# Kernel optimization log

Measured on AMD Instinct MI355X. Metric: run time of the kernel, lower is better.

Reference implementation:

```python
import jax, jax.numpy as jnp
import numpy as np

L = 0.05  # lx = ly = lz box half-extent

# 8 box corners [8,3]
_CORNERS = jnp.array([[sx * L, sy * L, sz * L]
                      for sx in (-1.0, 1.0) for sy in (-1.0, 1.0) for sz in (-1.0, 1.0)],
                     dtype=jnp.float32)
# match original ordering: [-,-,-],[-,-,+],[-,+,-],... which the comprehension above yields


def _euler_R(pose):
    """pose: [B,6] -> R [B,3,3], t [B,3] (yaw, pitch, roll convention from source)."""
    yaw, pitch, roll = pose[:, 0], pose[:, 1], pose[:, 2]
    cy, sy = jnp.cos(yaw), jnp.sin(yaw)
    cp, sp = jnp.cos(pitch), jnp.sin(pitch)
    cr, sr = jnp.cos(roll), jnp.sin(roll)
    R = jnp.stack([
        jnp.stack([cy * cp, cy * sp * sr - sy * cr, cy * sp * cr + sy * sr], axis=-1),
        jnp.stack([sy * cp, sy * sp * sr + cy * cr, sy * sp * cr - cy * sr], axis=-1),
        jnp.stack([-sp, cp * sr, cp * cr], axis=-1),
    ], axis=-2)  # [B,3,3]
    t = pose[:, 3:]  # [B,3]
    return R, t


def _transform_corners(pose):
    R, t = _euler_R(pose)
    # [B,8,3] = corners @ R^T + t
    return jnp.einsum('bij,nj->bni', R, _CORNERS) + t[:, None, :]


def setup_inputs() -> dict:
    key = jax.random.key(0)
    k1, k2, k3, k4 = jax.random.split(key, 4)
    B, C = 1048576, 16
    return {
        'pred_pose': jax.random.normal(k1, (B, 6), dtype=jnp.float32),
        'pred_class': jax.random.normal(k2, (B, C), dtype=jnp.float32),
        'target_pose': jax.random.normal(k3, (B, 6), dtype=jnp.float32),
        'target_class': jax.random.normal(k4, (B, C), dtype=jnp.float32),
    }


def reference(pred_pose, pred_class, target_pose, target_class):
    pts_pred = _transform_corners(pred_pose)    # [B,8,3]
    pts_gt = _transform_corners(target_pose)    # [B,8,3]
    # per-sample pose diff: mean over 8 corner L2 norms, then mean over batch
    norms = jnp.linalg.norm(pts_pred - pts_gt, axis=-1)  # [B,8]
    loss_pose = norms.mean(axis=-1).mean()
    class_loss = jnp.mean((pred_class - target_class) ** 2)
    total_loss = loss_pose + class_loss
    return total_loss, loss_pose, class_loss
```

## Files before the change

### kernel.cpp

```cpp
#include <hip/hip_runtime.h>
#include <math.h>

#define CORNER_L 0.05f

typedef float f4 __attribute__((ext_vector_type(4)));

constexpr int THREADS = 256;
constexpr int GROUPS  = 1024;
constexpr int CQ = 3, PQ = 2;
constexpr int CBLOCKS = CQ * GROUPS;
constexpr int PBLOCKS = PQ * GROUPS;
constexpr int TOTAL_BLOCKS = CBLOCKS + PBLOCKS;

__device__ __forceinline__ float pose_elem(
    float py, float pp_, float pr, float ptx, float pty, float ptz,
    float ty, float tp_, float tr, float ttx, float tty, float ttz)
{
    float sy1 = __sinf(py),  cy1 = __cosf(py);
    float sp1 = __sinf(pp_), cp1 = __cosf(pp_);
    float sr1 = __sinf(pr),  cr1 = __cosf(pr);
    float sy2 = __sinf(ty),  cy2 = __cosf(ty);
    float sp2 = __sinf(tp_), cp2 = __cosf(tp_);
    float sr2 = __sinf(tr),  cr2 = __cosf(tr);

    float a0 = CORNER_L * (cy1 * cp1 - cy2 * cp2);
    float a1 = CORNER_L * ((cy1 * sp1 * sr1 - sy1 * cr1) - (cy2 * sp2 * sr2 - sy2 * cr2));
    float a2 = CORNER_L * ((cy1 * sp1 * cr1 + sy1 * sr1) - (cy2 * sp2 * cr2 + sy2 * sr2));
    float b0 = CORNER_L * (sy1 * cp1 - sy2 * cp2);
    float b1 = CORNER_L * ((sy1 * sp1 * sr1 + cy1 * cr1) - (sy2 * sp2 * sr2 + cy2 * cr2));
    float b2 = CORNER_L * ((sy1 * sp1 * cr1 - cy1 * sr1) - (sy2 * sp2 * cr2 - cy2 * sr2));
    float c0 = CORNER_L * (sp2 - sp1);
    float c1 = CORNER_L * (cp1 * sr1 - cp2 * sr2);
    float c2 = CORNER_L * (cp1 * cr1 - cp2 * cr2);
    float dtx = ptx - ttx;
    float dty = pty - tty;
    float dtz = ptz - ttz;

    float nsum = 0.0f;
    #pragma unroll
    for (int s = 0; s < 8; ++s) {
        float sx = (s & 4) ? 1.0f : -1.0f;
        float sy = (s & 2) ? 1.0f : -1.0f;
        float sz = (s & 1) ? 1.0f : -1.0f;
        float d0 = sx * a0 + sy * a1 + sz * a2 + dtx;
        float d1 = sx * b0 + sy * b1 + sz * b2 + dty;
        float d2 = sx * c0 + sy * c1 + sz * c2 + dtz;
        nsum += __builtin_amdgcn_sqrtf(d0 * d0 + d1 * d1 + d2 * d2);
    }
    return nsum;
}

__global__ __launch_bounds__(THREADS) void pose_loss_fused(
    const f4* __restrict__ pp4, const f4* __restrict__ pc4,
    const f4* __restrict__ tp4, const f4* __restrict__ tc4,
    float* __restrict__ ws, int n4)
{
    const int tid = threadIdx.x;
    const int g   = blockIdx.x;
    const int grp = g / 5;
    const int r   = g - grp * 5;

    float acc = 0.0f;
    int out_idx;

    if (r < CQ) {
        const int cb = grp * CQ + r;
        const size_t G = (size_t)CBLOCKS * THREADS;
        for (size_t i = (size_t)cb * THREADS + tid; i < (size_t)n4; i += G) {
            f4 p = __builtin_nontemporal_load(pc4 + i);
            f4 t = __builtin_nontemporal_load(tc4 + i);
            f4 d = p - t;
            acc += d.x * d.x + d.y * d.y + d.z * d.z + d.w * d.w;
        }
        out_idx = cb;
    } else {
        const int pb = grp * PQ + (r - CQ);
        const size_t gtid = (size_t)pb * THREADS + tid;
        const size_t f = gtid * 3;
        f4 P0 = __builtin_nontemporal_load(pp4 + f);
        f4 P1 = __builtin_nontemporal_load(pp4 + f + 1);
        f4 P2 = __builtin_nontemporal_load(pp4 + f + 2);
        f4 T0 = __builtin_nontemporal_load(tp4 + f);
        f4 T1 = __builtin_nontemporal_load(tp4 + f + 1);
        f4 T2 = __builtin_nontemporal_load(tp4 + f + 2);
        acc += pose_elem(P0.x, P0.y, P0.z, P0.w, P1.x, P1.y,
                         T0.x, T0.y, T0.z, T0.w, T1.x, T1.y);
        acc += pose_elem(P1.z, P1.w, P2.x, P2.y, P2.z, P2.w,
                         T1.z, T1.w, T2.x, T2.y, T2.z, T2.w);
        out_idx = CBLOCKS + pb;
    }

    #pragma unroll
    for (int off = 32; off > 0; off >>= 1) acc += __shfl_down(acc, off);
    __shared__ float red[4];
    const int lane = tid & 63, wave = tid >> 6;
    if (lane == 0) red[wave] = acc;
    __syncthreads();
    if (tid == 0) ws[out_idx] = red[0] + red[1] + red[2] + red[3];
}

__global__ __launch_bounds__(THREADS) void pose_loss_finalize(
    const float* __restrict__ ws, float* __restrict__ out,
    float inv_pose, float inv_class)
{
    float c = 0.0f, p = 0.0f;
    for (int k = threadIdx.x; k < CBLOCKS; k += THREADS) c += ws[k];
    for (int k = threadIdx.x; k < PBLOCKS; k += THREADS) p += ws[CBLOCKS + k];
    #pragma unroll
    for (int off = 32; off > 0; off >>= 1) {
        p += __shfl_down(p, off);
        c += __shfl_down(c, off);
    }
    __shared__ float r_p[4], r_c[4];
    const int lane = threadIdx.x & 63, wave = threadIdx.x >> 6;
    if (lane == 0) { r_p[wave] = p; r_c[wave] = c; }
    __syncthreads();
    if (threadIdx.x == 0) {
        float lp = (r_p[0] + r_p[1] + r_p[2] + r_p[3]) * inv_pose;
        float lc = (r_c[0] + r_c[1] + r_c[2] + r_c[3]) * inv_class;
        out[0] = lp + lc;
        out[1] = lp;
        out[2] = lc;
    }
}

extern "C" void kernel_launch(void* const* d_in, const int* in_sizes, int n_in,
                              void* d_out, int out_size, void* d_ws, size_t ws_size,
                              hipStream_t stream) {
    const f4* pred_pose    = (const f4*)d_in[0];
    const f4* pred_class   = (const f4*)d_in[1];
    const f4* target_pose  = (const f4*)d_in[2];
    const f4* target_class = (const f4*)d_in[3];
    float* out = (float*)d_out;
    float* ws  = (float*)d_ws;

    const int B  = in_sizes[0] / 6;
    const int n4 = B * 4;

    pose_loss_fused<<<TOTAL_BLOCKS, THREADS, 0, stream>>>(
        pred_pose, pred_class, target_pose, target_class, ws, n4);

    const float inv_pose  = 1.0f / (8.0f  * (float)B);
    const float inv_class = 1.0f / (16.0f * (float)B);
    pose_loss_finalize<<<1, THREADS, 0, stream>>>(ws, out, inv_pose, inv_class);
}
```

Measured before the change: 174.6 us.

## Fuse finalize into main kernel via last-block atomic counter, unroll class loop

Removes the separate finalize kernel launch: each block writes its partial sum, fences, and bumps an atomic counter, and the last block to arrive does the final reduction and writes the outputs. A memset resets the counter before each launch. The class-loss loop is also unrolled by two with independent accumulators to get more loads in flight. The change trades one kernel launch for a memset op, an atomic per block and a serialized tail in the last block.

After: 425.8 us. +143.8%, slower.

```diff
diff --git a/kernel.cpp b/kernel.cpp
--- a/kernel.cpp
+++ b/kernel.cpp
@@ -53,7 +53,8 @@
 __global__ __launch_bounds__(THREADS) void pose_loss_fused(
     const f4* __restrict__ pp4, const f4* __restrict__ pc4,
     const f4* __restrict__ tp4, const f4* __restrict__ tc4,
-    float* __restrict__ ws, int n4)
+    float* __restrict__ ws, float* __restrict__ out,
+    int n4, float inv_pose, float inv_class)
 {
     const int tid = threadIdx.x;
     const int g   = blockIdx.x;
@@ -66,12 +67,20 @@
     if (r < CQ) {
         const int cb = grp * CQ + r;
         const size_t G = (size_t)CBLOCKS * THREADS;
-        for (size_t i = (size_t)cb * THREADS + tid; i < (size_t)n4; i += G) {
-            f4 p = __builtin_nontemporal_load(pc4 + i);
-            f4 t = __builtin_nontemporal_load(tc4 + i);
-            f4 d = p - t;
-            acc += d.x * d.x + d.y * d.y + d.z * d.z + d.w * d.w;
+        float acc1 = 0.0f;
+        for (size_t i = (size_t)cb * THREADS + tid; i < (size_t)n4; i += 2 * G) {
+            f4 p0 = __builtin_nontemporal_load(pc4 + i);
+            f4 t0 = __builtin_nontemporal_load(tc4 + i);
+            if (i + G < (size_t)n4) {
+                f4 p1 = __builtin_nontemporal_load(pc4 + i + G);
+                f4 t1 = __builtin_nontemporal_load(tc4 + i + G);
+                f4 d1 = p1 - t1;
+                acc1 += d1.x * d1.x + d1.y * d1.y + d1.z * d1.z + d1.w * d1.w;
+            }
+            f4 d0 = p0 - t0;
+            acc += d0.x * d0.x + d0.y * d0.y + d0.z * d0.z + d0.w * d0.w;
         }
+        acc += acc1;
         out_idx = cb;
     } else {
         const int pb = grp * PQ + (r - CQ);
@@ -96,31 +105,36 @@
     const int lane = tid & 63, wave = tid >> 6;
     if (lane == 0) red[wave] = acc;
     __syncthreads();
-    if (tid == 0) ws[out_idx] = red[0] + red[1] + red[2] + red[3];
-}
 
-__global__ __launch_bounds__(THREADS) void pose_loss_finalize(
-    const float* __restrict__ ws, float* __restrict__ out,
-    float inv_pose, float inv_class)
-{
-    float c = 0.0f, p = 0.0f;
-    for (int k = threadIdx.x; k < CBLOCKS; k += THREADS) c += ws[k];
-    for (int k = threadIdx.x; k < PBLOCKS; k += THREADS) p += ws[CBLOCKS + k];
-    #pragma unroll
-    for (int off = 32; off > 0; off >>= 1) {
-        p += __shfl_down(p, off);
-        c += __shfl_down(c, off);
+    __shared__ bool s_last;
+    if (tid == 0) {
+        ws[out_idx] = red[0] + red[1] + red[2] + red[3];
+        __threadfence();
+        unsigned old = atomicAdd((unsigned*)(ws + TOTAL_BLOCKS), 1u);
+        s_last = (old == (unsigned)(TOTAL_BLOCKS - 1));
     }
-    __shared__ float r_p[4], r_c[4];
-    const int lane = threadIdx.x & 63, wave = threadIdx.x >> 6;
-    if (lane == 0) { r_p[wave] = p; r_c[wave] = c; }
     __syncthreads();
-    if (threadIdx.x == 0) {
-        float lp = (r_p[0] + r_p[1] + r_p[2] + r_p[3]) * inv_pose;
-        float lc = (r_c[0] + r_c[1] + r_c[2] + r_c[3]) * inv_class;
-        out[0] = lp + lc;
-        out[1] = lp;
-        out[2] = lc;
+
+    if (s_last) {
+        __threadfence();
+        float c = 0.0f, p = 0.0f;
+        for (int k = tid; k < CBLOCKS; k += THREADS) c += ws[k];
+        for (int k = tid; k < PBLOCKS; k += THREADS) p += ws[CBLOCKS + k];
+        #pragma unroll
+        for (int off = 32; off > 0; off >>= 1) {
+            p += __shfl_down(p, off);
+            c += __shfl_down(c, off);
+        }
+        __shared__ float r_p[4], r_c[4];
+        if (lane == 0) { r_p[wave] = p; r_c[wave] = c; }
+        __syncthreads();
+        if (tid == 0) {
+            float lp = (r_p[0] + r_p[1] + r_p[2] + r_p[3]) * inv_pose;
+            float lc = (r_c[0] + r_c[1] + r_c[2] + r_c[3]) * inv_class;
+            out[0] = lp + lc;
+            out[1] = lp;
+            out[2] = lc;
+        }
     }
 }
 
@@ -137,10 +151,12 @@
     const int B  = in_sizes[0] / 6;
     const int n4 = B * 4;
 
-    pose_loss_fused<<<TOTAL_BLOCKS, THREADS, 0, stream>>>(
-        pred_pose, pred_class, target_pose, target_class, ws, n4);
+    hipMemsetAsync(ws + TOTAL_BLOCKS, 0, sizeof(unsigned), stream);
 
     const float inv_pose  = 1.0f / (8.0f  * (float)B);
     const float inv_class = 1.0f / (16.0f * (float)B);
-    pose_loss_finalize<<<1, THREADS, 0, stream>>>(ws, out, inv_pose, inv_class);
+
+    pose_loss_fused<<<TOTAL_BLOCKS, THREADS, 0, stream>>>(
+        pred_pose, pred_class, target_pose, target_class, ws, out,
+        n4, inv_pose, inv_class);
 }
```
